# Performance work log

Measured on AMD Instinct MI355X. Metric: run time of the kernel, lower is better.

Reference implementation:

```python
import jax, jax.numpy as jnp
import numpy as np

THETA = 10.0      # spike threshold
TAU_SR = 10.0     # synaptic (psp) alpha-kernel time constant
TAU_REF = 1.0     # refractory alpha-kernel time constant
SCALE_REF = 2.0   # refractory kernel scale (refKernel = -2*theta*alpha)
TS = 1.0          # simulation step


def psp(x):
    """SLAYER psp: causal conv along time with alpha kernel k[n] = (n*Ts/tau)*exp(1 - n*Ts/tau),
    realized exactly as a 2-state linear IIR recurrence. x: (..., T)."""
    a = jnp.float32(np.exp(-TS / TAU_SR))
    c = jnp.float32(np.e * TS / TAU_SR)
    xt = jnp.moveaxis(x, -1, 0)  # (T, ...)
    z = jnp.zeros_like(xt[0])

    def step(carry, xin):
        p, q = carry
        q = a * q + a * p          # q[n] = sum_m x[m]*(n-m)*a^(n-m)
        p = a * p + xin            # p[n] = sum_m x[m]*a^(n-m)
        return (p, q), c * q       # k-convolution output (k[0] = 0)

    _, y = jax.lax.scan(step, (z, z), xt)
    return jnp.moveaxis(y, 0, -1)


def spike(x):
    """SLAYER spike: threshold with refractory feedback. At each step the membrane is
    psp input plus -2*theta * (alpha-kernel conv of past spikes); spike amplitude 1/Ts = 1.
    Refractory alpha kernel realized with the same 2-state IIR. x: (..., T)."""
    a = jnp.float32(np.exp(-TS / TAU_REF))
    c = jnp.float32(np.e * TS / TAU_REF)
    xt = jnp.moveaxis(x, -1, 0)
    z = jnp.zeros_like(xt[0])

    def step(carry, ut):
        p, q = carry
        q = a * q + a * p
        u = ut - SCALE_REF * THETA * c * q   # membrane = input psp + refractory response
        s = (u >= THETA).astype(ut.dtype)
        p = a * p + s                        # spike feeds refractory state (k[0]=0 so no self-effect)
        return (p, q), s

    _, y = jax.lax.scan(step, (z, z), xt)
    return jnp.moveaxis(y, 0, -1)


def conv_t(x, w, pad):
    """Per-timestep 2D conv: x (B,Cin,H,W,T), w (Cout,Cin,k,k); time folded into batch."""
    b, cin, h, wd, t = x.shape
    xt = jnp.moveaxis(x, -1, 1).reshape(b * t, cin, h, wd)
    y = jax.lax.conv_general_dilated(xt, w, (1, 1), [(pad, pad), (pad, pad)])
    y = y.reshape(b, t, y.shape[1], y.shape[2], y.shape[3])
    return jnp.moveaxis(y, 1, -1)


def pool2(x):
    """SLAYER pool: zero-pad odd dims, 2x2 sum with constant weight 1.1*theta, stride 2."""
    b, ch, h, wd, t = x.shape
    ph, pw = (-h) % 2, (-wd) % 2
    x = jnp.pad(x, ((0, 0), (0, 0), (0, ph), (0, pw), (0, 0)))
    h2, w2 = (h + ph) // 2, (wd + pw) // 2
    x = x.reshape(b, ch, h2, 2, w2, 2, t).sum(axis=(3, 5))
    return 1.1 * THETA * x


def setup_inputs() -> dict:
    key = jax.random.key(0)
    ks = jax.random.split(key, 6)
    B, T = 4, 300
    s_in = (jax.random.uniform(ks[0], (B, 2, 34, 34, T)) < 0.03).astype(jnp.float32)
    def w(k, shape, scale):
        fan_in = int(np.prod(shape[1:]))
        return jax.random.normal(k, shape, jnp.float32) * (scale / np.sqrt(fan_in))
    return {
        "s_in": s_in,
        "Wc1": w(ks[1], (24, 2, 5, 5), 10.0),    # weightScale=10
        "Wc2": w(ks[2], (48, 24, 3, 3), 15.0),   # weightScale=15
        "Wc3": w(ks[3], (96, 48, 3, 3), 15.0),   # weightScale=15
        "Wd4a": w(ks[4], (256, 96, 5, 5), 1.0),
        "Wd4b": w(ks[5], (10, 256), 1.0),
    }


def reference(s_in, Wc1, Wc2, Wc3, Wd4a, Wd4b):
    x = spike(psp(conv_t(s_in, Wc1, 2)))                  # (B,24,34,34,T)
    x = spike(psp(pool2(x)))                              # (B,24,17,17,T)
    x = spike(psp(conv_t(x, Wc2, 1)))                     # (B,48,17,17,T)
    x = spike(psp(pool2(x)))                              # (B,48,9,9,T)
    x = spike(psp(conv_t(x, Wc3, 1)))                     # (B,96,9,9,T)
    x = spike(psp(pool2(x)))                              # (B,96,5,5,T)
    x = spike(psp(jnp.einsum('bchwt,ochw->bot', x, Wd4a)))  # (B,256,T)
    x = spike(psp(jnp.einsum('bnt,on->bot', x, Wd4b)))      # (B,10,T)
    return x
```

## Files before the change

kernel.cpp:

```cpp
#include <hip/hip_runtime.h>


#define TT 300

#define A1 0.9048374180359595f
#define C1 0.2718281828459045f
#define A2 0.36787944117144233f
#define C2 2.718281828459045f
#define KREF (20.0f * C2)
#define THETA_F 10.0f

typedef float v2f __attribute__((ext_vector_type(2)));
typedef float f32x4 __attribute__((ext_vector_type(4)));
typedef short bf16x8 __attribute__((ext_vector_type(8)));

struct IIR {
  float p1, q1, p2, q2;
  __device__ IIR() : p1(0.f), q1(0.f), p2(0.f), q2(0.f) {}
  __device__ inline float step(float xin) {
    q1 = A1 * q1 + A1 * p1;
    float y = C1 * q1;
    p1 = A1 * p1 + xin;
    q2 = A2 * q2 + A2 * p2;
    float u = y - KREF * q2;
    float s = (u >= THETA_F) ? 1.0f : 0.0f;
    p2 = A2 * p2 + s;
    return s;
  }
};

__global__ __launch_bounds__(256) void transpose_rc(const float* __restrict__ in,
                                                    float* __restrict__ out,
                                                    int R, int C) {
  __shared__ float tile[64][65];
  int c0 = blockIdx.x * 64, r0 = blockIdx.y * 64;
  int tx = threadIdx.x & 63, ty = threadIdx.x >> 6;
  for (int i = ty; i < 64; i += 4) {
    int r = r0 + i, c = c0 + tx;
    if (r < R && c < C) tile[i][tx] = in[(long)r * C + c];
  }
  __syncthreads();
  for (int i = ty; i < 64; i += 4) {
    int c = c0 + i, r = r0 + tx;
    if (c < C && r < R) out[(long)c * R + r] = tile[tx][i];
  }
}

__device__ inline unsigned rne_bf16_bits(float f) {
  unsigned u = __float_as_uint(f);
  return (u + 0x7FFFu + ((u >> 16) & 1u)) >> 16;
}
template <int CIN, int KS, int CO, int MT, int KC>
__global__ __launch_bounds__(256) void prep_mfma(const float* __restrict__ Wc,
                                                 ushort* __restrict__ Wm) {
  constexpr int K = CIN * KS * KS;
  constexpr int PLANE = MT * KC * 512;
  int i = blockIdx.x * 256 + threadIdx.x;
  if (i >= PLANE) return;
  int e = i & 7, l = (i >> 3) & 63;
  int rest = i >> 9;
  int kc = rest % KC, m = rest / KC;
  int co = m * 16 + (l & 15);
  int k = kc * 32 + (l >> 4) * 8 + e;
  float w = 0.f;
  if (k < K && co < CO) {
    int ci = k / (KS * KS), r = k % (KS * KS), dy = r / KS, dx = r % KS;
    w = Wc[((co * CIN + ci) * KS + dy) * KS + dx];
  }
  unsigned b0 = rne_bf16_bits(w);
  float f0 = __uint_as_float(b0 << 16);
  float d1 = w - f0;
  unsigned b1 = rne_bf16_bits(d1);
  float f1 = __uint_as_float(b1 << 16);
  unsigned b2 = rne_bf16_bits(d1 - f1);
  Wm[i] = (ushort)b0;
  Wm[PLANE + i] = (ushort)b1;
  Wm[2 * PLANE + i] = (ushort)b2;
}

template <int CIN, int HW, int KS, int PAD, int CO, int RS, int NW, int NSUB>
__global__ __launch_bounds__(NW * 64) void conv_mfma_d(const float* __restrict__ S,
                                                       const ushort* __restrict__ Wm,
                                                       float* __restrict__ U) {
  constexpr int PH = HW + 2 * PAD;
  constexpr int K = CIN * KS * KS;
  constexpr int KC = (K + 31) / 32;
  constexpr int MT = (CO + 15) / 16;
  constexpr int N = HW * HW;
  constexpr int NT = (N + 15) / 16;
  constexpr int NG = (NT + NSUB - 1) / NSUB;
  constexpr int TILE = CIN * PH * RS;
  constexpr int KPAD = KC * 32;
  __shared__ float lin[TILE];
  __shared__ int koff[KPAD];
  const int t = blockIdx.x, b = blockIdx.y, B = gridDim.y;
  const int tid = threadIdx.x;

  for (int i = tid; i < TILE; i += NW * 64) lin[i] = 0.f;
  for (int k = tid; k < KPAD; k += NW * 64) {
    int ci = k / (KS * KS), r = k % (KS * KS), dy = r / KS, dx = r % KS;
    koff[k] = (k < K) ? (ci * PH * RS + dy * RS + dx) : 0;
  }
  __syncthreads();
  const float* src = S + ((long)t * B + b) * (CIN * N);
  for (int i = tid; i < CIN * N; i += NW * 64) {
    int ci = i / N, r = i % N, iy = r / HW, ix = r % HW;
    lin[ci * PH * RS + (iy + PAD) * RS + ix + PAD] = src[i];
  }
  __syncthreads();

  const int lane = tid & 63;
  const int wv = tid >> 6;
  const int g = lane >> 4;
  const int col = lane & 15;

  bf16x8 af[3 * MT * KC];
#pragma unroll
  for (int f = 0; f < 3 * MT * KC; ++f)
    af[f] = *(const bf16x8*)(Wm + (long)f * 512 + lane * 8);

  for (int grp = wv; grp < NG; grp += NW) {
    const int px0 = grp * (16 * NSUB);
    bool vs[NSUB];
    int pxb[NSUB];
    bf16x8 bf[NSUB][KC];
#pragma unroll
    for (int s = 0; s < NSUB; ++s) {
      int px = px0 + s * 16 + col;
      vs[s] = px < N;
      int ppx = vs[s] ? px : 0;
      int y = ppx / HW, x = ppx % HW;
      pxb[s] = y * RS + x;
#pragma unroll
      for (int kc = 0; kc < KC; ++kc) {
        bf16x8 v;
#pragma unroll
        for (int e = 0; e < 8; ++e) {
          float val = lin[pxb[s] + koff[kc * 32 + g * 8 + e]];
          v[e] = (short)(__float_as_uint(val) >> 16);
        }
        bf[s][kc] = v;
      }
    }

#pragma unroll
    for (int m = 0; m < MT; ++m) {
      f32x4 acc[NSUB];
#pragma unroll
      for (int s = 0; s < NSUB; ++s) acc[s] = (f32x4){0.f, 0.f, 0.f, 0.f};
#pragma unroll
      for (int p = 0; p < 3; ++p) {
#pragma unroll
        for (int kc = 0; kc < KC; ++kc) {
          bf16x8 a = af[(p * MT + m) * KC + kc];
#pragma unroll
          for (int s = 0; s < NSUB; ++s)
            acc[s] = __builtin_amdgcn_mfma_f32_16x16x32_bf16(a, bf[s][kc], acc[s], 0, 0, 0);
        }
      }
      const int co0 = m * 16 + g * 4;
#pragma unroll
      for (int s = 0; s < NSUB; ++s) {
        if (vs[s]) {
          float* up = U + (((long)t * B + b) * CO + co0) * N + px0 + s * 16 + col;
#pragma unroll
          for (int j = 0; j < 4; ++j)
            if (co0 + j < CO) up[(long)j * N] = acc[s][j];
        }
      }
    }
  }
}

template <int CIN, int HW, int KS, int PAD, int CO, int RS, int NW, int MCHUNK>
__global__ __launch_bounds__(NW * 64) void conv_mfma_c(const float* __restrict__ S,
                                                       const ushort* __restrict__ Wm,
                                                       float* __restrict__ U) {
  constexpr int PH = HW + 2 * PAD;
  constexpr int K = CIN * KS * KS;
  constexpr int KC = (K + 31) / 32;
  constexpr int MT = CO / 16;
  constexpr int N = HW * HW;
  constexpr int NT = (N + 15) / 16;
  constexpr int TILE = CIN * PH * RS;
  constexpr int KPAD = KC * 32;
  constexpr int NCH = MT / MCHUNK;
  constexpr int CROWS = MCHUNK * 16;
  __shared__ float lin[TILE];
  __shared__ int koff[KPAD];
  __shared__ float cst[CROWS * N];
  const int t = blockIdx.x, b = blockIdx.y, B = gridDim.y;
  const int tid = threadIdx.x;

  for (int i = tid; i < TILE; i += NW * 64) lin[i] = 0.f;
  for (int k = tid; k < KPAD; k += NW * 64) {
    int ci = k / (KS * KS), r = k % (KS * KS), dy = r / KS, dx = r % KS;
    koff[k] = (k < K) ? (ci * PH * RS + dy * RS + dx) : 0;
  }
  __syncthreads();
  const float* src = S + ((long)t * B + b) * (CIN * N);
  for (int i = tid; i < CIN * N; i += NW * 64) {
    int ci = i / N, r = i % N, iy = r / HW, ix = r % HW;
    lin[ci * PH * RS + (iy + PAD) * RS + ix + PAD] = src[i];
  }
  __syncthreads();

  const int lane = tid & 63;
  const int wv = tid >> 6;
  const int g = lane >> 4;
  const int col = lane & 15;

  for (int ch = blockIdx.z; ch < NCH; ch += gridDim.z) {
    for (int nt = wv; nt < NT; nt += NW) {
      int px = nt * 16 + col;
      bool vpx = px < N;
      int ppx = vpx ? px : 0;
      int y = ppx / HW, x = ppx % HW;
      const int pxbase = y * RS + x;

      bf16x8 bf[KC];
#pragma unroll
      for (int kc = 0; kc < KC; ++kc) {
        bf16x8 v;
#pragma unroll
        for (int e = 0; e < 8; ++e) {
          float val = lin[pxbase + koff[kc * 32 + g * 8 + e]];
          v[e] = (short)(__float_as_uint(val) >> 16);
        }
        bf[kc] = v;
      }

#pragma unroll
      for (int ml = 0; ml < MCHUNK; ++ml) {
        const int m = ch * MCHUNK + ml;
        f32x4 acc = {0.f, 0.f, 0.f, 0.f};
#pragma unroll
        for (int p = 0; p < 3; ++p) {
#pragma unroll
          for (int kc = 0; kc < KC; ++kc) {
            bf16x8 a = *(const bf16x8*)(Wm + ((long)(p * MT + m) * KC + kc) * 512 + lane * 8);
            acc = __builtin_amdgcn_mfma_f32_16x16x32_bf16(a, bf[kc], acc, 0, 0, 0);
          }
        }
        if (vpx) {
          const int r0 = ml * 16 + g * 4;
#pragma unroll
          for (int j = 0; j < 4; ++j) cst[(r0 + j) * N + px] = acc[j];
        }
      }
    }
    __syncthreads();
    const f32x4* cs = (const f32x4*)cst;
    f32x4* ug = (f32x4*)(U + (((long)t * B + b) * CO + ch * CROWS) * N);
    for (int i = tid; i < CROWS * N / 4; i += NW * 64) ug[i] = cs[i];
    __syncthreads();
  }
}

template <int C, int HIN, int HOUT>
__global__ __launch_bounds__(128) void ppp4_tm(const float* __restrict__ U,
                                               float* __restrict__ out, int B) {
  const int NOUT = B * C * HOUT * HOUT;
  const long SIN = (long)B * C * HIN * HIN;
  int id = blockIdx.x * 128 + threadIdx.x;
  int sub = id & 3, m = id >> 2;
  bool active = m < NOUT;
  int mm = active ? m : 0;
  int x2 = mm % HOUT;
  int y2 = (mm / HOUT) % HOUT;
  int c = (mm / (HOUT * HOUT)) % C;
  int b = mm / (C * HOUT * HOUT);
  int iy = 2 * y2 + (sub >> 1), ix = 2 * x2 + (sub & 1);
  bool valid = active && iy < HIN && ix < HIN;
  const float* base = U + ((long)(b * C + c) * HIN + iy) * HIN + ix;
  bool writer = active && (sub == 0);
  float* op = out + mm;
  IIR si, so;
  float pr0 = valid ? base[0] : 0.f;
  float pr1 = valid ? base[SIN] : 0.f;
  float pr2 = valid ? base[2 * SIN] : 0.f;
  float pr3 = valid ? base[3 * SIN] : 0.f;
  for (int tb = 0; tb < TT; tb += 4) {
    float a0 = pr0, a1 = pr1, a2 = pr2, a3 = pr3;
    const float* nb = base + (long)(tb + 4) * SIN;
    pr0 = valid ? nb[0] : 0.f;
    pr1 = valid ? nb[SIN] : 0.f;
    pr2 = valid ? nb[2 * SIN] : 0.f;
    pr3 = valid ? nb[3 * SIN] : 0.f;
    {
      float s = si.step(a0);
      float v = s + __shfl_xor(s, 1); v += __shfl_xor(v, 2);
      float o = so.step(11.0f * v);
      if (writer) op[(long)tb * NOUT] = o;
    }
    {
      float s = si.step(a1);
      float v = s + __shfl_xor(s, 1); v += __shfl_xor(v, 2);
      float o = so.step(11.0f * v);
      if (writer) op[(long)(tb + 1) * NOUT] = o;
    }
    {
      float s = si.step(a2);
      float v = s + __shfl_xor(s, 1); v += __shfl_xor(v, 2);
      float o = so.step(11.0f * v);
      if (writer) op[(long)(tb + 2) * NOUT] = o;
    }
    {
      float s = si.step(a3);
      float v = s + __shfl_xor(s, 1); v += __shfl_xor(v, 2);
      float o = so.step(11.0f * v);
      if (writer) op[(long)(tb + 3) * NOUT] = o;
    }
  }
}

__global__ __launch_bounds__(256) void dense7k(const float* __restrict__ S,
                                               const float* __restrict__ Wt,
                                               float* __restrict__ P) {
  const int r0 = blockIdx.x * 16 + (threadIdx.x >> 6) * 4;
  const int kz = blockIdx.y;
  const int lane = threadIdx.x & 63;
  const float* s0 = S + (long)r0 * 2400;
  const float* s1 = s0 + 2400;
  const float* s2 = s0 + 4800;
  const float* s3 = s0 + 7200;
  const float* wp = Wt + lane * 4;
  v2f aA[4], aB[4];
#pragma unroll
  for (int o = 0; o < 4; ++o) { aA[o] = (v2f)(0.f); aB[o] = (v2f)(0.f); }
  const int k0 = kz * 300, k1 = k0 + 300;
  for (int k = k0; k < k1; k += 4) {
    float4 a0 = *(const float4*)(s0 + k);
    float4 a1 = *(const float4*)(s1 + k);
    float4 a2 = *(const float4*)(s2 + k);
    float4 a3 = *(const float4*)(s3 + k);
#define DSTEP(KK, AX)                                                        \
    {                                                                        \
      float4 w = *(const float4*)(wp + (long)(k + KK) * 256);                \
      v2f pA, pB;                                                            \
      pA.x = a0.AX; pA.y = a1.AX; pB.x = a2.AX; pB.y = a3.AX;                \
      aA[0] += pA * w.x; aA[1] += pA * w.y; aA[2] += pA * w.z; aA[3] += pA * w.w; \
      aB[0] += pB * w.x; aB[1] += pB * w.y; aB[2] += pB * w.z; aB[3] += pB * w.w; \
    }
    DSTEP(0, x) DSTEP(1, y) DSTEP(2, z) DSTEP(3, w)
#undef DSTEP
  }
  float* p = P + (long)kz * 307200 + (long)r0 * 256 + lane * 4;
#pragma unroll
  for (int o = 0; o < 4; ++o) p[o] = aA[o].x;
#pragma unroll
  for (int o = 0; o < 4; ++o) p[256 + o] = aA[o].y;
#pragma unroll
  for (int o = 0; o < 4; ++o) p[512 + o] = aB[o].x;
#pragma unroll
  for (int o = 0; o < 4; ++o) p[768 + o] = aB[o].y;
}

__global__ __launch_bounds__(256) void reduce8(const float* __restrict__ P,
                                               float* __restrict__ U7) {
  int i = blockIdx.x * 256 + threadIdx.x;
  if (i >= 76800) return;
  const float4* p = (const float4*)P;
  float4 a = p[i];
#pragma unroll
  for (int kz = 1; kz < 8; ++kz) {
    float4 b = p[(long)kz * 76800 + i];
    a.x += b.x; a.y += b.y; a.z += b.z; a.w += b.w;
  }
  ((float4*)U7)[i] = a;
}

__global__ __launch_bounds__(128) void psp7(const float* __restrict__ U7,
                                            float* __restrict__ out) {
  int n = blockIdx.x * 128 + threadIdx.x;
  IIR st;
  float pr0 = U7[n], pr1 = U7[1024 + n], pr2 = U7[2048 + n], pr3 = U7[3072 + n];
  for (int tb = 0; tb < TT; tb += 4) {
    float a0 = pr0, a1 = pr1, a2 = pr2, a3 = pr3;
    const float* nb = U7 + (long)(tb + 4) * 1024 + n;
    pr0 = nb[0]; pr1 = nb[1024]; pr2 = nb[2048]; pr3 = nb[3072];
    out[(long)tb * 1024 + n] = st.step(a0);
    out[(long)(tb + 1) * 1024 + n] = st.step(a1);
    out[(long)(tb + 2) * 1024 + n] = st.step(a2);
    out[(long)(tb + 3) * 1024 + n] = st.step(a3);
  }
}

__global__ __launch_bounds__(256) void dense8(const float* __restrict__ S,
                                              const float* __restrict__ W,
                                              float* __restrict__ U) {
  int id = blockIdx.x * 256 + threadIdx.x;
  if (id >= 12000) return;
  int o = id % 10, row = id / 10;
  const float* sr = S + (long)row * 256;
  const float* wr = W + o * 256;
  float acc = 0.f;
  for (int k = 0; k < 256; k += 4) {
    float4 a = *(const float4*)(sr + k);
    float4 w = *(const float4*)(wr + k);
    acc += a.x * w.x; acc += a.y * w.y; acc += a.z * w.z; acc += a.w * w.w;
  }
  U[id] = acc;
}

__global__ void psp8_out(const float* __restrict__ U, float* __restrict__ out) {
  int n = threadIdx.x;
  bool act = n < 40;
  int nn = act ? n : 0;
  IIR st;
  float pr0 = U[nn], pr1 = U[40 + nn], pr2 = U[80 + nn], pr3 = U[120 + nn];
  for (int tb = 0; tb < TT; tb += 4) {
    float a0 = pr0, a1 = pr1, a2 = pr2, a3 = pr3;
    const float* nb = U + (long)(tb + 4) * 40 + nn;
    pr0 = nb[0]; pr1 = nb[40]; pr2 = nb[80]; pr3 = nb[120];
    float o0 = st.step(a0), o1 = st.step(a1), o2 = st.step(a2), o3 = st.step(a3);
    if (act) {
      out[nn * TT + tb] = o0;
      out[nn * TT + tb + 1] = o1;
      out[nn * TT + tb + 2] = o2;
      out[nn * TT + tb + 3] = o3;
    }
  }
}

extern "C" void kernel_launch(void* const* d_in, const int* in_sizes, int n_in,
                              void* d_out, int out_size, void* d_ws, size_t ws_size,
                              hipStream_t stream) {
  const float* s_in = (const float*)d_in[0];
  const float* Wc1  = (const float*)d_in[1];
  const float* Wc2  = (const float*)d_in[2];
  const float* Wc3  = (const float*)d_in[3];
  const float* Wd4a = (const float*)d_in[4];
  const float* Wd4b = (const float*)d_in[5];

  float* Buf1 = (float*)d_ws;
  float* Buf2 = Buf1 + 33292800;
  float* s2   = Buf2;
  float* s4   = Buf2 + 8323200;
  float* Wt4a = Buf2 + 12988800;
  float* T0   = Buf2 + 13910400;
  float* s7   = Buf2 + 16737840;
  float* P7   = Buf2 + 17045040;
  float* U7   = Buf2 + 19502640;
  float* s6   = Buf2;
  float* U8   = Buf1;
  ushort* Wm1 = (ushort*)P7;
  ushort* Wm2 = Wm1 + 18432;
  ushort* Wm3 = Wm1 + 50688;

  transpose_rc<<<dim3(5, 145), 256, 0, stream>>>(s_in, T0, 9248, 300);
  transpose_rc<<<dim3(38, 4), 256, 0, stream>>>(Wd4a, Wt4a, 256, 2400);
  prep_mfma<2, 5, 24, 2, 2><<<24, 256, 0, stream>>>(Wc1, Wm1);
  prep_mfma<24, 3, 48, 3, 7><<<42, 256, 0, stream>>>(Wc2, Wm2);
  prep_mfma<48, 3, 96, 6, 14><<<168, 256, 0, stream>>>(Wc3, Wm3);

  conv_mfma_d<2, 34, 5, 2, 24, 39, 8, 4><<<dim3(300, 4), 512, 0, stream>>>(T0, Wm1, Buf1);
  ppp4_tm<24, 34, 17><<<867, 128, 0, stream>>>(Buf1, s2, 4);
  conv_mfma_c<24, 17, 3, 1, 48, 19, 8, 1><<<dim3(300, 4), 512, 0, stream>>>(s2, Wm2, Buf1);
  ppp4_tm<48, 17, 9><<<486, 128, 0, stream>>>(Buf1, s4, 4);
  conv_mfma_c<48, 9, 3, 1, 96, 13, 6, 3><<<dim3(300, 4, 2), 384, 0, stream>>>(s4, Wm3, Buf1);
  ppp4_tm<96, 9, 5><<<300, 128, 0, stream>>>(Buf1, s6, 4);
  dense7k<<<dim3(75, 8), 256, 0, stream>>>(s6, Wt4a, P7);
  reduce8<<<300, 256, 0, stream>>>(P7, U7);
  psp7<<<8, 128, 0, stream>>>(U7, s7);
  dense8<<<47, 256, 0, stream>>>(s7, Wd4b, U8);
  psp8_out<<<1, 64, 0, stream>>>(U8, (float*)d_out);
}
```

Before: 602.0 us.

## Use channel-last bf16 shared tile for vectorized conv B-operand loads

The conv2/conv3 MFMA kernels now stage the input tile in shared memory as bf16 in channel-last (HWC) layout, and the weight prep reorders K as (dy,dx,ci). Each 8-element B fragment then comes from a single 16-byte LDS load at a precomputed offset instead of eight scalar gathered loads through a koff table with per-element truncation. This cuts LDS traffic, shared-memory footprint and address arithmetic. It relies on groups of 8 consecutive k never crossing a channel boundary (CIN multiples of 8), and the padded CPAD is needed to keep the wide loads aligned and in bounds.

```diff
diff --git a/kernel.cpp b/kernel.cpp
--- a/kernel.cpp
+++ b/kernel.cpp
@@ -50,7 +50,7 @@
   unsigned u = __float_as_uint(f);
   return (u + 0x7FFFu + ((u >> 16) & 1u)) >> 16;
 }
-template <int CIN, int KS, int CO, int MT, int KC>
+template <int CIN, int KS, int CO, int MT, int KC, int CL>
 __global__ __launch_bounds__(256) void prep_mfma(const float* __restrict__ Wc,
                                                  ushort* __restrict__ Wm) {
   constexpr int K = CIN * KS * KS;
@@ -64,7 +64,18 @@
   int k = kc * 32 + (l >> 4) * 8 + e;
   float w = 0.f;
   if (k < K && co < CO) {
-    int ci = k / (KS * KS), r = k % (KS * KS), dy = r / KS, dx = r % KS;
+    int ci, dy, dx;
+    if (CL) {
+      ci = k % CIN;
+      int r = k / CIN;
+      dy = r / KS;
+      dx = r % KS;
+    } else {
+      ci = k / (KS * KS);
+      int r = k % (KS * KS);
+      dy = r / KS;
+      dx = r % KS;
+    }
     w = Wc[((co * CIN + ci) * KS + dy) * KS + dx];
   }
   unsigned b0 = rne_bf16_bits(w);
@@ -172,36 +183,40 @@
   }
 }
 
-template <int CIN, int HW, int KS, int PAD, int CO, int RS, int NW, int MCHUNK>
-__global__ __launch_bounds__(NW * 64) void conv_mfma_c(const float* __restrict__ S,
+template <int CIN, int HW, int KS, int PAD, int CO, int CPAD, int NW, int MCHUNK>
+__global__ __launch_bounds__(NW * 64) void conv_mfma_v(const float* __restrict__ S,
                                                        const ushort* __restrict__ Wm,
                                                        float* __restrict__ U) {
-  constexpr int PH = HW + 2 * PAD;
+  constexpr int PW = HW + 2 * PAD;
   constexpr int K = CIN * KS * KS;
   constexpr int KC = (K + 31) / 32;
+  constexpr int KPAD = KC * 32;
+  constexpr int RMAX = (KPAD - 1) / CIN;
+  constexpr int DYMAX = RMAX / KS;
+  constexpr int PHA = (HW + DYMAX > PW) ? (HW + DYMAX) : PW;
   constexpr int MT = CO / 16;
   constexpr int N = HW * HW;
   constexpr int NT = (N + 15) / 16;
-  constexpr int TILE = CIN * PH * RS;
-  constexpr int KPAD = KC * 32;
   constexpr int NCH = MT / MCHUNK;
   constexpr int CROWS = MCHUNK * 16;
-  __shared__ float lin[TILE];
-  __shared__ int koff[KPAD];
+  __shared__ ushort linb[PHA * PW * CPAD];
+  __shared__ int offb[KC * 4];
   __shared__ float cst[CROWS * N];
   const int t = blockIdx.x, b = blockIdx.y, B = gridDim.y;
   const int tid = threadIdx.x;
 
-  for (int i = tid; i < TILE; i += NW * 64) lin[i] = 0.f;
-  for (int k = tid; k < KPAD; k += NW * 64) {
-    int ci = k / (KS * KS), r = k % (KS * KS), dy = r / KS, dx = r % KS;
-    koff[k] = (k < K) ? (ci * PH * RS + dy * RS + dx) : 0;
+  for (int i = tid; i < PHA * PW * CPAD / 2; i += NW * 64) ((int*)linb)[i] = 0;
+  for (int i = tid; i < KC * 4; i += NW * 64) {
+    int k0 = (i >> 2) * 32 + (i & 3) * 8;
+    int ci0 = k0 % CIN, r0 = k0 / CIN;
+    offb[i] = ((r0 / KS) * PW + (r0 % KS)) * CPAD + ci0;
   }
   __syncthreads();
   const float* src = S + ((long)t * B + b) * (CIN * N);
   for (int i = tid; i < CIN * N; i += NW * 64) {
     int ci = i / N, r = i % N, iy = r / HW, ix = r % HW;
-    lin[ci * PH * RS + (iy + PAD) * RS + ix + PAD] = src[i];
+    linb[((iy + PAD) * PW + ix + PAD) * CPAD + ci] =
+        (ushort)(__float_as_uint(src[i]) >> 16);
   }
   __syncthreads();
 
@@ -209,6 +224,10 @@
   const int wv = tid >> 6;
   const int g = lane >> 4;
   const int col = lane & 15;
+
+  int boff[KC];
+#pragma unroll
+  for (int kc = 0; kc < KC; ++kc) boff[kc] = offb[kc * 4 + g];
 
   for (int ch = blockIdx.z; ch < NCH; ch += gridDim.z) {
     for (int nt = wv; nt < NT; nt += NW) {
@@ -216,19 +235,12 @@
       bool vpx = px < N;
       int ppx = vpx ? px : 0;
       int y = ppx / HW, x = ppx % HW;
-      const int pxbase = y * RS + x;
+      const int pxb = (y * PW + x) * CPAD;
 
       bf16x8 bf[KC];
 #pragma unroll
-      for (int kc = 0; kc < KC; ++kc) {
-        bf16x8 v;
-#pragma unroll
-        for (int e = 0; e < 8; ++e) {
-          float val = lin[pxbase + koff[kc * 32 + g * 8 + e]];
-          v[e] = (short)(__float_as_uint(val) >> 16);
-        }
-        bf[kc] = v;
-      }
+      for (int kc = 0; kc < KC; ++kc)
+        bf[kc] = *(const bf16x8*)(linb + pxb + boff[kc]);
 
 #pragma unroll
       for (int ml = 0; ml < MCHUNK; ++ml) {
@@ -450,15 +462,15 @@
 
   transpose_rc<<<dim3(5, 145), 256, 0, stream>>>(s_in, T0, 9248, 300);
   transpose_rc<<<dim3(38, 4), 256, 0, stream>>>(Wd4a, Wt4a, 256, 2400);
-  prep_mfma<2, 5, 24, 2, 2><<<24, 256, 0, stream>>>(Wc1, Wm1);
-  prep_mfma<24, 3, 48, 3, 7><<<42, 256, 0, stream>>>(Wc2, Wm2);
-  prep_mfma<48, 3, 96, 6, 14><<<168, 256, 0, stream>>>(Wc3, Wm3);
+  prep_mfma<2, 5, 24, 2, 2, 0><<<24, 256, 0, stream>>>(Wc1, Wm1);
+  prep_mfma<24, 3, 48, 3, 7, 1><<<42, 256, 0, stream>>>(Wc2, Wm2);
+  prep_mfma<48, 3, 96, 6, 14, 1><<<168, 256, 0, stream>>>(Wc3, Wm3);
 
   conv_mfma_d<2, 34, 5, 2, 24, 39, 8, 4><<<dim3(300, 4), 512, 0, stream>>>(T0, Wm1, Buf1);
   ppp4_tm<24, 34, 17><<<867, 128, 0, stream>>>(Buf1, s2, 4);
-  conv_mfma_c<24, 17, 3, 1, 48, 19, 8, 1><<<dim3(300, 4), 512, 0, stream>>>(s2, Wm2, Buf1);
+  conv_mfma_v<24, 17, 3, 1, 48, 24, 8, 1><<<dim3(300, 4), 512, 0, stream>>>(s2, Wm2, Buf1);
   ppp4_tm<48, 17, 9><<<486, 128, 0, stream>>>(Buf1, s4, 4);
-  conv_mfma_c<48, 9, 3, 1, 96, 13, 6, 3><<<dim3(300, 4, 2), 384, 0, stream>>>(s4, Wm3, Buf1);
+  conv_mfma_v<48, 9, 3, 1, 96, 56, 6, 3><<<dim3(300, 4, 2), 384, 0, stream>>>(s4, Wm3, Buf1);
   ppp4_tm<96, 9, 5><<<300, 128, 0, stream>>>(Buf1, s6, 4);
   dense7k<<<dim3(75, 8), 256, 0, stream>>>(s6, Wt4a, P7);
   reduce8<<<300, 256, 0, stream>>>(P7, U7);
```

Result: faster. 554.2 us, median of 2 (-7.9%).
